# Optimization experiments

Measured on AMD Instinct MI355X. Metric: run time of the kernel, lower is better.

The kernel has to match this reference:

```python
import jax, jax.numpy as jnp
import numpy as np

B, S, D, H, DFF = 2, 2048, 768, 12, 3072
HD = D // H
LN_EPS = 1e-5


def _layernorm(x, g, b):
    mu = jnp.mean(x, axis=-1, keepdims=True)
    var = jnp.mean((x - mu) ** 2, axis=-1, keepdims=True)
    return (x - mu) * jax.lax.rsqrt(var + LN_EPS) * g + b


def setup_inputs() -> dict:
    key = jax.random.key(0)
    ks = jax.random.split(key, 16)
    s_d = 1.0 / np.sqrt(D)
    s_ff = 1.0 / np.sqrt(DFF)
    return {
        "x": jax.random.normal(ks[0], (B, S, D), jnp.float32),
        "alibi_bias": jax.random.normal(ks[1], (H, S, S), jnp.float32) * 0.1,
        "Wq": jax.random.normal(ks[2], (D, D), jnp.float32) * s_d,
        "bq": jnp.zeros((D,), jnp.float32),
        "Wk": jax.random.normal(ks[3], (D, D), jnp.float32) * s_d,
        "bk": jnp.zeros((D,), jnp.float32),
        "Wv": jax.random.normal(ks[4], (D, D), jnp.float32) * s_d,
        "bv": jnp.zeros((D,), jnp.float32),
        "Wo": jax.random.normal(ks[5], (D, D), jnp.float32) * s_d,
        "bo": jnp.zeros((D,), jnp.float32),
        "W1": jax.random.normal(ks[6], (D, DFF), jnp.float32) * s_d,
        "b1": jnp.zeros((DFF,), jnp.float32),
        "W2": jax.random.normal(ks[7], (DFF, D), jnp.float32) * s_ff,
        "b2": jnp.zeros((D,), jnp.float32),
        "g1": jnp.ones((D,), jnp.float32),
        "be1": jnp.zeros((D,), jnp.float32),
        "g2": jnp.ones((D,), jnp.float32),
        "be2": jnp.zeros((D,), jnp.float32),
    }


def reference(x, alibi_bias, Wq, bq, Wk, bk, Wv, bv, Wo, bo, W1, b1, W2, b2, g1, be1, g2, be2):
    # QKV projections -> (B, H, S, HD)
    def split_heads(t):
        return t.reshape(B, S, H, HD).transpose(0, 2, 1, 3)

    q = split_heads(x @ Wq + bq)
    k = split_heads(x @ Wk + bk)
    v = split_heads(x @ Wv + bv)

    # causal mask (S, S): -inf above diagonal
    causal = jnp.where(jnp.triu(jnp.ones((S, S), bool), k=1), -jnp.inf, 0.0).astype(x.dtype)
    mask = alibi_bias[None] + causal[None, None]  # (1, H, S, S) broadcast over batch

    scale = 1.0 / np.sqrt(HD)
    scores = jnp.einsum("bhqd,bhkd->bhqk", q, k) * scale + mask
    probs = jax.nn.softmax(scores, axis=-1)
    attn = jnp.einsum("bhqk,bhkd->bhqd", probs, v)  # (B, H, S, HD)
    attn = attn.transpose(0, 2, 1, 3).reshape(B, S, D)
    attn = attn @ Wo + bo

    x = _layernorm(x + attn, g1, be1)
    ff = jax.nn.relu(x @ W1 + b1) @ W2 + b2
    x = _layernorm(x + ff, g2, be2)
    return x
```

## Files before the change

### kernel.cpp

```cpp
#include <hip/hip_runtime.h>
#include <hip/hip_bf16.h>

#define BB 2
#define SS 2048
#define DD 768
#define HH 12
#define HD 64
#define DFF 3072
#define NROW (BB * SS)
#define QLD  2304
#define LN_EPS 1e-5f
#define NSPLIT 4

typedef __attribute__((ext_vector_type(8))) short bf16x8;
typedef __attribute__((ext_vector_type(4))) short bf16x4;
typedef __attribute__((ext_vector_type(4))) float f32x4;

__device__ __forceinline__ void gll16(const void* g, void* l) {
    __builtin_amdgcn_global_load_lds(
        (const __attribute__((address_space(1))) unsigned int*)g,
        (__attribute__((address_space(3))) unsigned int*)l,
        16, 0, 0);
}

__device__ __forceinline__ unsigned short bf16bits(float f) {
    __hip_bfloat16 h = __float2bfloat16(f);
    return *(unsigned short*)&h;
}

__device__ __forceinline__ float bf16tof(unsigned short u) {
    unsigned int ui = ((unsigned int)u) << 16;
    return __uint_as_float(ui);
}

__device__ __forceinline__ float block_sum(float v, float* red) {
    __syncthreads();
    #pragma unroll
    for (int off = 32; off > 0; off >>= 1) v += __shfl_down(v, off, 64);
    if ((threadIdx.x & 63) == 0) red[threadIdx.x >> 6] = v;
    __syncthreads();
    if (threadIdx.x == 0) red[0] = red[0] + red[1] + red[2] + red[3];
    __syncthreads();
    return red[0];
}

template<int TM, int TN>
__global__ __launch_bounds__(256) void mfma_gemm(
        const __hip_bfloat16* __restrict__ A, const __hip_bfloat16* __restrict__ BT,
        const float* __restrict__ bias, float* __restrict__ Cf,
        __hip_bfloat16* __restrict__ Cb,
        int N, int K, int relu, int bf16out, int qscale_cols) {
    constexpr int BK = 64;
    constexpr int MW = TM / 32;
    constexpr int NW = TN / 32;
    __shared__ __hip_bfloat16 a_s[TM * BK];
    __shared__ __hip_bfloat16 b_s[TN * BK];

    const int tid  = threadIdx.x;
    const int lane = tid & 63;
    const int wid  = tid >> 6;
    const int wm   = (wid & 1) * (TM / 2);
    const int wn   = (wid >> 1) * (TN / 2);
    const int qq   = lane & 15;
    const int quad = lane >> 4;
    const int m0 = blockIdx.y * TM;
    const int n0 = blockIdx.x * TN;

    const int r8   = lane >> 3;
    const int u8   = lane & 7;
    const int gcol = ((u8 ^ r8) << 3);

    f32x4 acc[MW][NW] = {};

    for (int k0 = 0; k0 < K; k0 += BK) {
        const __hip_bfloat16* Ag = A + (size_t)m0 * K + k0 + gcol;
        #pragma unroll
        for (int i = 0; i < TM / 32; i++) {
            const int row = i * 32 + wid * 8 + r8;
            gll16(Ag + (size_t)row * K, a_s + row * BK + u8 * 8);
        }
        const __hip_bfloat16* Bg = BT + (size_t)n0 * K + k0 + gcol;
        #pragma unroll
        for (int i = 0; i < TN / 32; i++) {
            const int row = i * 32 + wid * 8 + r8;
            gll16(Bg + (size_t)row * K, b_s + row * BK + u8 * 8);
        }
        __syncthreads();

        #pragma unroll
        for (int kh = 0; kh < 2; kh++) {
            const int ku = kh * 4 + quad;
            bf16x8 af[MW], bfr[NW];
            #pragma unroll
            for (int mi = 0; mi < MW; mi++) {
                const int row = wm + mi * 16 + qq;
                af[mi] = *(const bf16x8*)(a_s + row * BK + ((ku ^ (qq & 7)) << 3));
            }
            #pragma unroll
            for (int ni = 0; ni < NW; ni++) {
                const int row = wn + ni * 16 + qq;
                bfr[ni] = *(const bf16x8*)(b_s + row * BK + ((ku ^ (qq & 7)) << 3));
            }
            #pragma unroll
            for (int mi = 0; mi < MW; mi++)
                #pragma unroll
                for (int ni = 0; ni < NW; ni++)
                    acc[mi][ni] = __builtin_amdgcn_mfma_f32_16x16x32_bf16(
                            af[mi], bfr[ni], acc[mi][ni], 0, 0, 0);
        }
        __syncthreads();
    }

    #pragma unroll
    for (int mi = 0; mi < MW; mi++) {
        #pragma unroll
        for (int ni = 0; ni < NW; ni++) {
            const int col = n0 + wn + ni * 16 + qq;
            const float bv = bias[col];
            const float sc = (col < qscale_cols) ? 0.125f : 1.0f;
            #pragma unroll
            for (int r = 0; r < 4; r++) {
                const int row = m0 + wm + mi * 16 + quad * 4 + r;
                float v = acc[mi][ni][r] + bv;
                if (relu) v = fmaxf(v, 0.f);
                v *= sc;
                if (bf16out) Cb[(size_t)row * N + col] = __float2bfloat16(v);
                else         Cf[(size_t)row * N + col] = v;
            }
        }
    }
}

__device__ __forceinline__ void transpose_tile(
        const float* __restrict__ in, __hip_bfloat16* __restrict__ out,
        int K, int N, int tix, int tiy, float (*t)[33]) {
    const int n0 = tix * 32;
    const int k0 = tiy * 32;
    const int r = threadIdx.x >> 3;
    const int c = threadIdx.x & 7;
    float4 v = *(const float4*)&in[(size_t)(k0 + r) * N + n0 + c * 4];
    t[r][c * 4 + 0] = v.x;
    t[r][c * 4 + 1] = v.y;
    t[r][c * 4 + 2] = v.z;
    t[r][c * 4 + 3] = v.w;
    __syncthreads();
    union { unsigned short u[4]; uint2 w; } pk;
    #pragma unroll
    for (int j = 0; j < 4; j++) pk.u[j] = bf16bits(t[c * 4 + j][r]);
    *(uint2*)&out[(size_t)(n0 + r) * K + k0 + c * 4] = pk.w;
}

__global__ __launch_bounds__(256) void prep_kernel(
        const float* __restrict__ Wq, const float* __restrict__ Wk,
        const float* __restrict__ Wv, const float* __restrict__ Wo,
        const float* __restrict__ W1, const float* __restrict__ W2,
        const float* __restrict__ bq, const float* __restrict__ bk,
        const float* __restrict__ bv, const float* __restrict__ x,
        __hip_bfloat16* __restrict__ WqkvT, __hip_bfloat16* __restrict__ WoT,
        __hip_bfloat16* __restrict__ W1T, __hip_bfloat16* __restrict__ W2T,
        float* __restrict__ biasc, __hip_bfloat16* __restrict__ xb) {
    __shared__ float t[32][33];
    const int bx = blockIdx.x;
    if (bx < 2304) {
        const int wsel = bx / 576;
        const int r = bx - wsel * 576;
        const float* in = (wsel == 0) ? Wq : (wsel == 1) ? Wk : (wsel == 2) ? Wv : Wo;
        __hip_bfloat16* out = (wsel == 3) ? WoT : WqkvT + (size_t)wsel * DD * DD;
        transpose_tile(in, out, DD, DD, r % 24, r / 24, t);
    } else if (bx < 4608) {
        const int r = bx - 2304;
        transpose_tile(W1, W1T, DD, DFF, r % 96, r / 96, t);
    } else if (bx < 6912) {
        const int r = bx - 4608;
        transpose_tile(W2, W2T, DFF, DD, r % 24, r / 24, t);
    } else if (bx < 9984) {
        const int i = (bx - 6912) * 256 + threadIdx.x;
        float4 v = ((const float4*)x)[i];
        union { unsigned short u[4]; uint2 w; } pk;
        pk.u[0] = bf16bits(v.x); pk.u[1] = bf16bits(v.y);
        pk.u[2] = bf16bits(v.z); pk.u[3] = bf16bits(v.w);
        ((uint2*)xb)[i] = pk.w;
    } else {
        const int i = (bx - 9984) * 256 + threadIdx.x;
        if (i < QLD)
            biasc[i] = (i < DD) ? bq[i] : ((i < 2 * DD) ? bk[i - DD] : bv[i - 2 * DD]);
    }
}

__global__ __launch_bounds__(256) void flash_attn_kernel(
        const __hip_bfloat16* __restrict__ QKV, const float* __restrict__ alibi,
        __hip_bfloat16* __restrict__ Opart, float* __restrict__ ml) {
    const int qt = (int)(gridDim.x >> 2) - 1 - (int)(blockIdx.x >> 2);
    const int s  = blockIdx.x & 3;
    const int h  = blockIdx.y;
    const int b  = blockIdx.z;
    const int tid  = threadIdx.x;
    const int lane = tid & 63;
    const int w    = tid >> 6;
    const int qq   = lane & 15;
    const int quad = lane >> 4;
    const int q0   = qt * 64;

    __shared__ unsigned short K_s[64 * 72];
    __shared__ unsigned short V_t[64 * 72];
    __shared__ unsigned short P_t[4][16 * 72];

    const size_t qrow = ((size_t)(b * SS + q0 + w * 16 + qq)) * QLD + (size_t)h * HD;
    const bf16x8 qf0 = *(const bf16x8*)(QKV + qrow + quad * 8);
    const bf16x8 qf1 = *(const bf16x8*)(QKV + qrow + 32 + quad * 8);

    f32x4 O[4] = {};
    float m_i = -1e30f, l_i = 0.f;

    const float* alrow = alibi + ((size_t)h * SS + q0 + w * 16 + qq) * SS;
    const size_t kvrow0 = (size_t)(b * SS) * QLD + (size_t)h * HD + w * 16;
    const int lim = q0 + w * 16 + qq;

    for (int t = s; t * 64 <= q0; t += NSPLIT) {
        const int k0 = t * 64;
        __syncthreads();

        {
            const size_t kv = kvrow0 + (size_t)(k0 + lane) * QLD;
            bf16x8 kv0 = *(const bf16x8*)(QKV + DD + kv);
            bf16x8 kv1 = *(const bf16x8*)(QKV + DD + kv + 8);
            *(bf16x8*)&K_s[lane * 72 + w * 16]     = kv0;
            *(bf16x8*)&K_s[lane * 72 + w * 16 + 8] = kv1;
            bf16x8 vv0 = *(const bf16x8*)(QKV + 2 * DD + kv);
            bf16x8 vv1 = *(const bf16x8*)(QKV + 2 * DD + kv + 8);
            #pragma unroll
            for (int j = 0; j < 8; j++) {
                V_t[(w * 16 + j) * 72 + lane]     = vv0[j];
                V_t[(w * 16 + 8 + j) * 72 + lane] = vv1[j];
            }
        }
        __syncthreads();

        float4 av[4];
        #pragma unroll
        for (int c = 0; c < 4; c++)
            av[c] = *(const float4*)(alrow + k0 + c * 16 + quad * 4);

        __builtin_amdgcn_s_setprio(1);
        f32x4 S[4];
        #pragma unroll
        for (int c = 0; c < 4; c++) {
            f32x4 sacc = {};
            bf16x8 kf0 = *(const bf16x8*)&K_s[(c * 16 + qq) * 72 + quad * 8];
            bf16x8 kf1 = *(const bf16x8*)&K_s[(c * 16 + qq) * 72 + 32 + quad * 8];
            sacc = __builtin_amdgcn_mfma_f32_16x16x32_bf16(kf0, qf0, sacc, 0, 0, 0);
            sacc = __builtin_amdgcn_mfma_f32_16x16x32_bf16(kf1, qf1, sacc, 0, 0, 0);
            S[c] = sacc;
        }
        __builtin_amdgcn_s_setprio(0);

        float sv[16];
        float smax = -1e30f;
        const int klim = lim - k0;
        #pragma unroll
        for (int c = 0; c < 4; c++) {
            #pragma unroll
            for (int r = 0; r < 4; r++) {
                const int key = c * 16 + quad * 4 + r;
                float sc = S[c][r] + ((const float*)&av[c])[r];
                if (key > klim) sc = -1e30f;
                sv[c * 4 + r] = sc;
                smax = fmaxf(smax, sc);
            }
        }
        smax = fmaxf(smax, __shfl_xor(smax, 16));
        smax = fmaxf(smax, __shfl_xor(smax, 32));

        const float nm = fmaxf(m_i, smax);
        const float alpha = __expf(m_i - nm);
        float lsum = 0.f;
        #pragma unroll
        for (int i = 0; i < 16; i++) {
            const float e = __expf(sv[i] - nm);
            sv[i] = e;
            lsum += e;
        }
        lsum += __shfl_xor(lsum, 16);
        lsum += __shfl_xor(lsum, 32);
        l_i = l_i * alpha + lsum;
        m_i = nm;

        #pragma unroll
        for (int c = 0; c < 4; c++) {
            bf16x4 pk;
            #pragma unroll
            for (int r = 0; r < 4; r++) pk[r] = (short)bf16bits(sv[c * 4 + r]);
            *(bf16x4*)&P_t[w][qq * 72 + c * 16 + quad * 4] = pk;
        }

        #pragma unroll
        for (int r = 0; r < 4; r++) {
            const float ar = __shfl(alpha, quad * 4 + r);
            #pragma unroll
            for (int d = 0; d < 4; d++) O[d][r] *= ar;
        }

        const bf16x8 pf0 = *(const bf16x8*)&P_t[w][qq * 72 + quad * 8];
        const bf16x8 pf1 = *(const bf16x8*)&P_t[w][qq * 72 + 32 + quad * 8];
        __builtin_amdgcn_s_setprio(1);
        #pragma unroll
        for (int d0 = 0; d0 < 4; d0++) {
            bf16x8 vf0 = *(const bf16x8*)&V_t[(d0 * 16 + qq) * 72 + quad * 8];
            bf16x8 vf1 = *(const bf16x8*)&V_t[(d0 * 16 + qq) * 72 + 32 + quad * 8];
            O[d0] = __builtin_amdgcn_mfma_f32_16x16x32_bf16(pf0, vf0, O[d0], 0, 0, 0);
            O[d0] = __builtin_amdgcn_mfma_f32_16x16x32_bf16(pf1, vf1, O[d0], 0, 0, 0);
        }
        __builtin_amdgcn_s_setprio(0);
    }

    if (quad == 0) {
        float* mlp = ml + (((size_t)(b * SS + q0 + w * 16 + qq) * HH + h) * NSPLIT + s) * 2;
        mlp[0] = m_i;
        mlp[1] = l_i;
    }
    #pragma unroll
    for (int r = 0; r < 4; r++) {
        const int row = q0 + w * 16 + quad * 4 + r;
        __hip_bfloat16* op = Opart +
            (((size_t)(b * SS + row) * HH + h) * NSPLIT + s) * 64 + qq;
        op[0]  = __float2bfloat16(O[0][r]);
        op[16] = __float2bfloat16(O[1][r]);
        op[32] = __float2bfloat16(O[2][r]);
        op[48] = __float2bfloat16(O[3][r]);
    }
}

__global__ __launch_bounds__(256) void attn_combine_kernel(
        const __hip_bfloat16* __restrict__ Opart, const float* __restrict__ ml,
        __hip_bfloat16* __restrict__ attnb) {
    const int idx = blockIdx.x * 256 + threadIdx.x;
    const int rr  = idx / 96;
    const int rem = idx - rr * 96;
    const int h   = rem >> 3;
    const int d8  = (rem & 7) * 8;
    const size_t base = ((size_t)rr * HH + h) * NSPLIT;
    float ms[NSPLIT], ls[NSPLIT];
    float m = -1e30f;
    #pragma unroll
    for (int s = 0; s < NSPLIT; s++) {
        ms[s] = ml[(base + s) * 2];
        ls[s] = ml[(base + s) * 2 + 1];
        m = fmaxf(m, ms[s]);
    }
    float es[NSPLIT], denom = 0.f;
    #pragma unroll
    for (int s = 0; s < NSPLIT; s++) {
        es[s] = __expf(ms[s] - m);
        denom += ls[s] * es[s];
    }
    const float inv = 1.f / denom;
    float acc[8] = {};
    #pragma unroll
    for (int s = 0; s < NSPLIT; s++) {
        const bf16x8 o = *(const bf16x8*)(Opart + (base + s) * 64 + d8);
        #pragma unroll
        for (int j = 0; j < 8; j++)
            acc[j] += bf16tof((unsigned short)o[j]) * es[s];
    }
    union { unsigned short u[8]; bf16x8 v; } pk;
    #pragma unroll
    for (int j = 0; j < 8; j++) pk.u[j] = bf16bits(acc[j] * inv);
    *(bf16x8*)(attnb + (size_t)rr * DD + h * 64 + d8) = pk.v;
}

__global__ __launch_bounds__(256) void ln_kernel(
        const float* __restrict__ a, const float* __restrict__ r,
        const float* __restrict__ g, const float* __restrict__ beta,
        float* __restrict__ outf, __hip_bfloat16* __restrict__ outb) {
    const int row = blockIdx.x;
    const int tid = threadIdx.x;
    __shared__ float red[64];

    float vals[3];
    float s = 0.f;
    #pragma unroll
    for (int i = 0; i < 3; i++) {
        const int col = i * 256 + tid;
        float t = a[(size_t)row * DD + col] + r[(size_t)row * DD + col];
        vals[i] = t;
        s += t;
    }
    const float mean = block_sum(s, red) * (1.f / DD);

    float s2 = 0.f;
    #pragma unroll
    for (int i = 0; i < 3; i++) {
        float d = vals[i] - mean;
        s2 += d * d;
    }
    const float var = block_sum(s2, red) * (1.f / DD);
    const float rstd = rsqrtf(var + LN_EPS);

    #pragma unroll
    for (int i = 0; i < 3; i++) {
        const int col = i * 256 + tid;
        const float o = (vals[i] - mean) * rstd * g[col] + beta[col];
        outf[(size_t)row * DD + col] = o;
        if (outb) outb[(size_t)row * DD + col] = __float2bfloat16(o);
    }
}

extern "C" void kernel_launch(void* const* d_in, const int* in_sizes, int n_in,
                              void* d_out, int out_size, void* d_ws, size_t ws_size,
                              hipStream_t stream) {
    const float* x     = (const float*)d_in[0];
    const float* alibi = (const float*)d_in[1];
    const float* Wq = (const float*)d_in[2];
    const float* bq = (const float*)d_in[3];
    const float* Wk = (const float*)d_in[4];
    const float* bk = (const float*)d_in[5];
    const float* Wv = (const float*)d_in[6];
    const float* bv = (const float*)d_in[7];
    const float* Wo = (const float*)d_in[8];
    const float* bo = (const float*)d_in[9];
    const float* W1 = (const float*)d_in[10];
    const float* b1 = (const float*)d_in[11];
    const float* W2 = (const float*)d_in[12];
    const float* b2 = (const float*)d_in[13];
    const float* g1 = (const float*)d_in[14];
    const float* be1 = (const float*)d_in[15];
    const float* g2 = (const float*)d_in[16];
    const float* be2 = (const float*)d_in[17];
    float* out = (float*)d_out;

    char* p = (char*)d_ws;
    auto alloc = [&](size_t bytes) { char* r = p; p += (bytes + 255) & ~(size_t)255; return r; };
    __hip_bfloat16* WqkvT = (__hip_bfloat16*)alloc((size_t)QLD * DD * 2);
    __hip_bfloat16* WoT   = (__hip_bfloat16*)alloc((size_t)DD * DD * 2);
    __hip_bfloat16* W1T   = (__hip_bfloat16*)alloc((size_t)DFF * DD * 2);
    __hip_bfloat16* W2T   = (__hip_bfloat16*)alloc((size_t)DD * DFF * 2);
    float*          biasc = (float*)alloc((size_t)QLD * 4);
    __hip_bfloat16* xb    = (__hip_bfloat16*)alloc((size_t)NROW * DD * 2);
    __hip_bfloat16* qkvb  = (__hip_bfloat16*)alloc((size_t)NROW * DFF * 2);
    __hip_bfloat16* attnb = (__hip_bfloat16*)alloc((size_t)NROW * DD * 2);
    float*          proj  = (float*)alloc((size_t)NROW * DD * 4);
    float*          ln1   = (float*)alloc((size_t)NROW * DD * 4);
    __hip_bfloat16* ln1b  = xb;
    __hip_bfloat16* ff1b  = qkvb;
    float*          ff2   = proj;

    __hip_bfloat16* Opart = (__hip_bfloat16*)proj;
    float*          mlbuf = (float*)xb;

    const dim3 blk(256);

    prep_kernel<<<dim3(9993), blk, 0, stream>>>(
            Wq, Wk, Wv, Wo, W1, W2, bq, bk, bv, x,
            WqkvT, WoT, W1T, W2T, biasc, xb);

    mfma_gemm<128, 128><<<dim3(QLD / 128, NROW / 128), blk, 0, stream>>>(
            xb, WqkvT, biasc, nullptr, qkvb, QLD, DD, 0, 1, DD);

    flash_attn_kernel<<<dim3(NSPLIT * (SS / 64), HH, BB), blk, 0, stream>>>(
            qkvb, alibi, Opart, mlbuf);
    attn_combine_kernel<<<dim3(NROW * 96 / 256), blk, 0, stream>>>(
            Opart, mlbuf, attnb);

    mfma_gemm<128, 64><<<dim3(DD / 64, NROW / 128), blk, 0, stream>>>(
            attnb, WoT, bo, proj, nullptr, DD, DD, 0, 0, 0);

    ln_kernel<<<dim3(NROW), blk, 0, stream>>>(x, proj, g1, be1, ln1, ln1b);

    mfma_gemm<128, 128><<<dim3(DFF / 128, NROW / 128), blk, 0, stream>>>(
            ln1b, W1T, b1, nullptr, ff1b, DFF, DD, 1, 1, 0);
    mfma_gemm<128, 64><<<dim3(DD / 64, NROW / 128), blk, 0, stream>>>(
            ff1b, W2T, b2, ff2, nullptr, DD, DFF, 0, 0, 0);

    ln_kernel<<<dim3(NROW), blk, 0, stream>>>(ln1, ff2, g2, be2, out, nullptr);
}
```

Baseline: 499.0 us.

## Double-buffer GEMM shared-memory tiles to overlap global loads with MFMA

The GEMM kernel now keeps two LDS buffers for the A and B tiles. It issues the global-to-LDS loads for the next K tile before computing on the current one, then uses explicit vmcnt waits so only the current tile's loads must finish. This is meant to hide global memory latency behind MFMA work instead of stalling at every K step. In exchange LDS use doubles, which may lower occupancy, and the hand-written waitcnt values depend on the exact count of loads in flight being correct.

```diff
diff --git a/kernel.cpp b/kernel.cpp
--- a/kernel.cpp
+++ b/kernel.cpp
@@ -53,8 +53,9 @@
     constexpr int BK = 64;
     constexpr int MW = TM / 32;
     constexpr int NW = TN / 32;
-    __shared__ __hip_bfloat16 a_s[TM * BK];
-    __shared__ __hip_bfloat16 b_s[TN * BK];
+    constexpr int LOADS = TM / 32 + TN / 32;
+    __shared__ __hip_bfloat16 a_s[2][TM * BK];
+    __shared__ __hip_bfloat16 b_s[2][TN * BK];
 
     const int tid  = threadIdx.x;
     const int lane = tid & 63;
@@ -70,23 +71,43 @@
     const int u8   = lane & 7;
     const int gcol = ((u8 ^ r8) << 3);
 
-    f32x4 acc[MW][NW] = {};
-
-    for (int k0 = 0; k0 < K; k0 += BK) {
+    auto stage = [&](int buf, int k0) {
         const __hip_bfloat16* Ag = A + (size_t)m0 * K + k0 + gcol;
         #pragma unroll
         for (int i = 0; i < TM / 32; i++) {
             const int row = i * 32 + wid * 8 + r8;
-            gll16(Ag + (size_t)row * K, a_s + row * BK + u8 * 8);
+            gll16(Ag + (size_t)row * K, &a_s[buf][row * BK + u8 * 8]);
         }
         const __hip_bfloat16* Bg = BT + (size_t)n0 * K + k0 + gcol;
         #pragma unroll
         for (int i = 0; i < TN / 32; i++) {
             const int row = i * 32 + wid * 8 + r8;
-            gll16(Bg + (size_t)row * K, b_s + row * BK + u8 * 8);
-        }
-        __syncthreads();
-
+            gll16(Bg + (size_t)row * K, &b_s[buf][row * BK + u8 * 8]);
+        }
+    };
+
+    f32x4 acc[MW][NW] = {};
+    const int NT = K / BK;
+
+    stage(0, 0);
+    int cur = 0;
+    for (int t = 0; t < NT; t++) {
+        if (t + 1 < NT) {
+            stage(cur ^ 1, (t + 1) * BK);
+            if constexpr (LOADS == 8)
+                asm volatile("s_waitcnt vmcnt(8)" ::: "memory");
+            else if constexpr (LOADS == 6)
+                asm volatile("s_waitcnt vmcnt(6)" ::: "memory");
+            else
+                asm volatile("s_waitcnt vmcnt(0)" ::: "memory");
+        } else {
+            asm volatile("s_waitcnt vmcnt(0)" ::: "memory");
+        }
+        __builtin_amdgcn_s_barrier();
+        __builtin_amdgcn_sched_barrier(0);
+
+        const __hip_bfloat16* as = a_s[cur];
+        const __hip_bfloat16* bs = b_s[cur];
         #pragma unroll
         for (int kh = 0; kh < 2; kh++) {
             const int ku = kh * 4 + quad;
@@ -94,12 +115,12 @@
             #pragma unroll
             for (int mi = 0; mi < MW; mi++) {
                 const int row = wm + mi * 16 + qq;
-                af[mi] = *(const bf16x8*)(a_s + row * BK + ((ku ^ (qq & 7)) << 3));
+                af[mi] = *(const bf16x8*)(as + row * BK + ((ku ^ (qq & 7)) << 3));
             }
             #pragma unroll
             for (int ni = 0; ni < NW; ni++) {
                 const int row = wn + ni * 16 + qq;
-                bfr[ni] = *(const bf16x8*)(b_s + row * BK + ((ku ^ (qq & 7)) << 3));
+                bfr[ni] = *(const bf16x8*)(bs + row * BK + ((ku ^ (qq & 7)) << 3));
             }
             #pragma unroll
             for (int mi = 0; mi < MW; mi++)
@@ -108,7 +129,10 @@
                     acc[mi][ni] = __builtin_amdgcn_mfma_f32_16x16x32_bf16(
                             af[mi], bfr[ni], acc[mi][ni], 0, 0, 0);
         }
-        __syncthreads();
+
+        __builtin_amdgcn_sched_barrier(0);
+        __builtin_amdgcn_s_barrier();
+        cur ^= 1;
     }
 
     #pragma unroll
```

Measured after the change: 518.9 us. 1.04x slower.
